# Optimization experiments

Hardware: AMD Instinct MI355X
Metric: run time of the kernel (lower is better)

The kernel has to match this reference:

```python
import jax, jax.numpy as jnp
import numpy as np

# Faithful JAX port of torchvision rotate(img, -angle, BILINEAR) applied to every
# (image, angle) pair, matching torchvision's align_corners=False grid_sample math:
# for output pixel (yo, xo), with a = radians(angle) (sign of the module's -angle
# already folded in), centered coords X = xo-(W-1)/2, Y = yo-(H-1)/2:
#   src_x = cos(a)*X - sin(a)*Y + (W-1)/2
#   src_y = sin(a)*X + cos(a)*Y + (H-1)/2
# then bilinear sample with zero padding outside the image.

def rotate_batch(image_batch, angles):
    n, c, H, W = image_batch.shape  # c == 1 (required by original output assignment)
    img = image_batch[:, 0]         # (n, H, W)
    a = jnp.deg2rad(angles)         # (k,)
    cx = (W - 1) * 0.5
    cy = (H - 1) * 0.5
    X = (jnp.arange(W, dtype=image_batch.dtype) - cx)[None, None, :]  # (1,1,W)
    Y = (jnp.arange(H, dtype=image_batch.dtype) - cy)[None, :, None]  # (1,H,1)
    ca = jnp.cos(a)[:, None, None]  # (k,1,1)
    sa = jnp.sin(a)[:, None, None]
    sx = ca * X - sa * Y + cx       # (k,H,W) source x in pixel coords
    sy = sa * X + ca * Y + cy       # (k,H,W)

    x0f = jnp.floor(sx); y0f = jnp.floor(sy)
    wx = sx - x0f; wy = sy - y0f    # bilinear fractional weights
    x0 = x0f.astype(jnp.int32); y0 = y0f.astype(jnp.int32)
    x1 = x0 + 1; y1 = y0 + 1

    def gather(yi, xi):
        # zero-padding grid_sample: out-of-bounds corners contribute 0
        valid = (yi >= 0) & (yi < H) & (xi >= 0) & (xi < W)      # (k,H,W)
        yc = jnp.clip(yi, 0, H - 1)
        xc = jnp.clip(xi, 0, W - 1)
        vals = img[:, yc, xc]                                     # (n,k,H,W)
        return jnp.where(valid[None], vals, jnp.zeros((), image_batch.dtype))

    out = (gather(y0, x0) * ((1 - wy) * (1 - wx))[None]
         + gather(y0, x1) * ((1 - wy) * wx)[None]
         + gather(y1, x0) * (wy * (1 - wx))[None]
         + gather(y1, x1) * (wy * wx)[None])
    return out  # (n, k, H, W)


def setup_inputs() -> dict:
    key = jax.random.key(0)
    k_img, k_ang = jax.random.split(key)
    image_batch = jax.random.normal(k_img, (32, 1, 512, 512), dtype=jnp.float32)
    angles = jax.random.uniform(k_ang, (8,), dtype=jnp.float32) * 360.0  # degrees
    return {"image_batch": image_batch, "angles": angles}


def reference(image_batch, angles):
    return rotate_batch(image_batch, angles)
```

## Files before the change

### kernel.cpp

```cpp
#include <hip/hip_runtime.h>
#include <math.h>
#include <stdint.h>

#define N_IMG 32
#define N_ANG 8
#define H_ 512
#define W_ 512

#define TX 64
#define TY 32
#define LP 84
#define NCHUNK 25
#define LWORDS (NCHUNK * 256)
#define OP 68

__global__ __launch_bounds__(256, 3) void rotate_tile_kernel(
    const float* __restrict__ img,
    const float* __restrict__ angles,
    float* __restrict__ out)
{
    __shared__ float tile[2 * LWORDS];

    const int bz   = blockIdx.z;
    const int k    = bz >> 1;
    const int n0   = (bz & 1) * (N_IMG / 2);
    const int tx0  = blockIdx.x * TX;
    const int ty0  = blockIdx.y * TY;
    const int tid  = threadIdx.x;
    const int wid  = tid >> 6;
    const int lane = tid & 63;

    const float rad = angles[k] * 0.017453292519943295f;
    float sa, ca;
    sincosf(rad, &sa, &ca);
    const float cx = (W_ - 1) * 0.5f;
    const float cy = (H_ - 1) * 0.5f;

    float minsx = 1e30f, maxsx = -1e30f, minsy = 1e30f, maxsy = -1e30f;
#pragma unroll
    for (int cyi = 0; cyi < 2; ++cyi) {
#pragma unroll
        for (int cxi = 0; cxi < 2; ++cxi) {
            const float xr = (float)(tx0 + cxi * (TX - 1)) - cx;
            const float yr = (float)(ty0 + cyi * (TY - 1)) - cy;
            const float sx = ca * xr - sa * yr + cx;
            const float sy = sa * xr + ca * yr + cy;
            minsx = fminf(minsx, sx); maxsx = fmaxf(maxsx, sx);
            minsy = fminf(minsy, sy); maxsy = fmaxf(maxsy, sy);
        }
    }
    const int bx0 = min(max((int)floorf(minsx) - 1, 0), W_ - 1);
    const int by0 = min(max((int)floorf(minsy) - 1, 0), H_ - 1);
    const int bx0m = (bx0 & ~3) - 4;
    const int by0m = by0 - 1;

    int goff[7];
    int nst = 0;
    for (int s = wid; s < NCHUNK; s += 4) {
        const int f   = s * 256 + lane * 4;
        const int row = f / LP;
        const int col = f - row * LP;
        const int grow = min(max(by0m + row, 0), H_ - 1);
        const int gcol = min(max(bx0m + col, 0), W_ - 4);
        goff[nst++] = grow * W_ + gcol;
    }

    const bool modeA = fabsf(ca) >= fabsf(sa);
    const int pxg = modeA ? (tid & 15) : (tid >> 4);
    const int py0 = modeA ? (tid >> 4) : (tid & 15);
    const int px  = pxg * 4;

    int   ob[2][4];
    float w00[2][4], w01[2][4], w10[2][4], w11[2][4];
#pragma unroll
    for (int p = 0; p < 2; ++p) {
        const int   yy = ty0 + py0 + p * 16;
        const float yr = (float)yy - cy;
#pragma unroll
        for (int j = 0; j < 4; ++j) {
            const int   xx = tx0 + px + j;
            const float xr = (float)xx - cx;
            const float sxs = ca * xr - sa * yr + cx;
            const float sys = sa * xr + ca * yr + cy;
            const float x0f = floorf(sxs), y0f = floorf(sys);
            const float wx = sxs - x0f, wy = sys - y0f;
            const int x0 = (int)x0f, y0 = (int)y0f;
            const bool vx0 = ((unsigned)x0       < (unsigned)W_);
            const bool vx1 = ((unsigned)(x0 + 1) < (unsigned)W_);
            const bool vy0 = ((unsigned)y0       < (unsigned)H_);
            const bool vy1 = ((unsigned)(y0 + 1) < (unsigned)H_);
            const int lx = min(max(x0 - bx0m, 0), 82);
            const int ly = min(max(y0 - by0m, 0), 74);
            ob[p][j] = ly * LP + lx;
            const float omwx = 1.0f - wx, omwy = 1.0f - wy;
            w00[p][j] = omwy * omwx * (float)(vy0 && vx0);
            w01[p][j] = omwy * wx   * (float)(vy0 && vx1);
            w10[p][j] = wy   * omwx * (float)(vy1 && vx0);
            w11[p][j] = wy   * wx   * (float)(vy1 && vx1);
        }
    }

    auto stage_img = [&](int n, int b) {
        const float* __restrict__ ib = img + (size_t)n * (H_ * W_);
        float* dst0 = &tile[b * LWORDS];
        for (int i = 0; i < nst; ++i) {
            __builtin_amdgcn_global_load_lds(
                (const __attribute__((address_space(1))) void*)(ib + goff[i]),
                (__attribute__((address_space(3))) void*)(dst0 + (wid + i * 4) * 256),
                16, 0, 0);
        }
    };

    stage_img(n0, 0);
    asm volatile("s_waitcnt vmcnt(0)" ::: "memory");
    __builtin_amdgcn_s_barrier();

    int cur = 0;
    for (int idx = 0; idx < N_IMG / 2; ++idx) {
        const int n = n0 + idx;
        const bool more = (idx + 1 < N_IMG / 2);
        if (more) {
            stage_img(n + 1, cur ^ 1);
            __builtin_amdgcn_sched_barrier(0);
        }

        const float* __restrict__ tb = &tile[cur * LWORDS];
        float* __restrict__ outn =
            out + ((size_t)(n * N_ANG + k) * H_ + ty0) * W_ + tx0;

        float v[2][4];
#pragma unroll
        for (int p = 0; p < 2; ++p) {
#pragma unroll
            for (int j = 0; j < 4; ++j) {
                const float* __restrict__ b0 = &tb[ob[p][j]];
                v[p][j] = w00[p][j] * b0[0]
                        + w01[p][j] * b0[1]
                        + w10[p][j] * b0[LP]
                        + w11[p][j] * b0[LP + 1];
            }
        }

        if (modeA) {
#pragma unroll
            for (int p = 0; p < 2; ++p) {
                float4* dst = (float4*)(outn + (py0 + p * 16) * W_ + px);
                *dst = make_float4(v[p][0], v[p][1], v[p][2], v[p][3]);
            }
        } else {
            __builtin_amdgcn_s_barrier();
            float* __restrict__ os = (float*)&tile[cur * LWORDS];
#pragma unroll
            for (int p = 0; p < 2; ++p) {
                float4* d = (float4*)(os + (py0 + p * 16) * OP + px);
                *d = make_float4(v[p][0], v[p][1], v[p][2], v[p][3]);
            }
            asm volatile("s_waitcnt lgkmcnt(0)" ::: "memory");
            __builtin_amdgcn_sched_barrier(0);
            __builtin_amdgcn_s_barrier();
            const int rx = (tid & 15) * 4;
            const int ry = tid >> 4;
#pragma unroll
            for (int p = 0; p < 2; ++p) {
                float4 t = *(float4*)(os + (ry + p * 16) * OP + rx);
                *(float4*)(outn + (ry + p * 16) * W_ + rx) = t;
            }
        }

        if (more) {
            asm volatile("s_waitcnt vmcnt(2)" ::: "memory");
            __builtin_amdgcn_s_barrier();
            cur ^= 1;
        }
    }
}

extern "C" void kernel_launch(void* const* d_in, const int* in_sizes, int n_in,
                              void* d_out, int out_size, void* d_ws, size_t ws_size,
                              hipStream_t stream) {
    const float* img    = (const float*)d_in[0];
    const float* angles = (const float*)d_in[1];
    float* out          = (float*)d_out;

    dim3 block(256, 1, 1);
    dim3 grid(W_ / TX, H_ / TY, N_ANG * 2);
    rotate_tile_kernel<<<grid, block, 0, stream>>>(img, angles, out);
}
```

Baseline: 339.3 us.

## Enlarge tiles, size LDS footprint per angle, and remap blocks across XCDs

The output tile grows from 64x32 to 64x64, and the LDS staging region is now sized from each tile's rotated bounding box instead of a fixed worst case. The double-buffered prefetch pipeline is replaced by a single buffer with a full wait per image, which frees LDS for four blocks per CU. Bilinear weights are recomputed from the fractional parts, with validity packed into bitmasks to cut register use. The grid is flattened to 1024 blocks and remapped so XCDs share angles and image halves. Output writes become nontemporal stores. The cost is that the overlap between loads and compute is lost.

```diff
diff --git a/kernel.cpp b/kernel.cpp
--- a/kernel.cpp
+++ b/kernel.cpp
@@ -8,24 +8,31 @@
 #define W_ 512
 
 #define TX 64
-#define TY 32
-#define LP 84
-#define NCHUNK 25
-#define LWORDS (NCHUNK * 256)
+#define TY 64
+#define MAXCH 37
+#define LDSW (MAXCH * 256)
 #define OP 68
 
-__global__ __launch_bounds__(256, 3) void rotate_tile_kernel(
+typedef float f32x4 __attribute__((ext_vector_type(4)));
+
+__global__ __launch_bounds__(256, 4) void rotate_tile_kernel(
     const float* __restrict__ img,
     const float* __restrict__ angles,
     float* __restrict__ out)
 {
-    __shared__ float tile[2 * LWORDS];
-
-    const int bz   = blockIdx.z;
-    const int k    = bz >> 1;
-    const int n0   = (bz & 1) * (N_IMG / 2);
-    const int tx0  = blockIdx.x * TX;
-    const int ty0  = blockIdx.y * TY;
+    __shared__ float tile[LDSW];
+
+    const int b    = blockIdx.x;
+    const int xcd  = b & 7;
+    const int slot = b >> 3;
+    const int sel  = slot & 1;
+    const int tnum = slot >> 1;
+    const int h    = xcd >> 2;
+    const int k    = (xcd & 3) + sel * 4;
+    const int n0   = h * (N_IMG / 2);
+    const int tx0  = (tnum & 7) * TX;
+    const int ty0  = (tnum >> 3) * TY;
+
     const int tid  = threadIdx.x;
     const int wid  = tid >> 6;
     const int lane = tid & 63;
@@ -51,14 +58,21 @@
     }
     const int bx0 = min(max((int)floorf(minsx) - 1, 0), W_ - 1);
     const int by0 = min(max((int)floorf(minsy) - 1, 0), H_ - 1);
-    const int bx0m = (bx0 & ~3) - 4;
-    const int by0m = by0 - 1;
-
-    int goff[7];
+    const int bx0m = (minsx < 0.0f) ? -4 : (bx0 & ~3);
+    const int by0m = (minsy < 0.0f) ? -1 : by0;
+    int cols  = (int)floorf(maxsx) + 2 - bx0m;
+    int LP    = (cols + 3) & ~3;
+    if ((LP & 7) == 0) LP += 4;
+    int rowsS = (int)floorf(maxsy) + 2 - by0m;
+    LP    = min(LP, 100);
+    rowsS = min(rowsS, 94);
+    const int nchunk = min((rowsS * LP + 255) >> 8, MAXCH);
+
+    int goff[10];
     int nst = 0;
-    for (int s = wid; s < NCHUNK; s += 4) {
-        const int f   = s * 256 + lane * 4;
-        const int row = f / LP;
+    for (int s = wid; s < nchunk; s += 4) {
+        const int f = s * 256 + lane * 4;
+        const int row = (int)((unsigned)f / (unsigned)LP);
         const int col = f - row * LP;
         const int grow = min(max(by0m + row, 0), H_ - 1);
         const int gcol = min(max(bx0m + col, 0), W_ - 4);
@@ -70,10 +84,11 @@
     const int py0 = modeA ? (tid >> 4) : (tid & 15);
     const int px  = pxg * 4;
 
-    int   ob[2][4];
-    float w00[2][4], w01[2][4], w10[2][4], w11[2][4];
-#pragma unroll
-    for (int p = 0; p < 2; ++p) {
+    int      obw[4][4];
+    float    wxv[4][4], wyv[4][4];
+    unsigned vm[2] = {0u, 0u};
+#pragma unroll
+    for (int p = 0; p < 4; ++p) {
         const int   yy = ty0 + py0 + p * 16;
         const float yr = (float)yy - cy;
 #pragma unroll
@@ -83,77 +98,88 @@
             const float sxs = ca * xr - sa * yr + cx;
             const float sys = sa * xr + ca * yr + cy;
             const float x0f = floorf(sxs), y0f = floorf(sys);
-            const float wx = sxs - x0f, wy = sys - y0f;
+            wxv[p][j] = sxs - x0f;
+            wyv[p][j] = sys - y0f;
             const int x0 = (int)x0f, y0 = (int)y0f;
-            const bool vx0 = ((unsigned)x0       < (unsigned)W_);
-            const bool vx1 = ((unsigned)(x0 + 1) < (unsigned)W_);
-            const bool vy0 = ((unsigned)y0       < (unsigned)H_);
-            const bool vy1 = ((unsigned)(y0 + 1) < (unsigned)H_);
-            const int lx = min(max(x0 - bx0m, 0), 82);
-            const int ly = min(max(y0 - by0m, 0), 74);
-            ob[p][j] = ly * LP + lx;
-            const float omwx = 1.0f - wx, omwy = 1.0f - wy;
-            w00[p][j] = omwy * omwx * (float)(vy0 && vx0);
-            w01[p][j] = omwy * wx   * (float)(vy0 && vx1);
-            w10[p][j] = wy   * omwx * (float)(vy1 && vx0);
-            w11[p][j] = wy   * wx   * (float)(vy1 && vx1);
-        }
-    }
-
-    auto stage_img = [&](int n, int b) {
+            const unsigned vx0 = ((unsigned)x0       < (unsigned)W_) ? 1u : 0u;
+            const unsigned vx1 = ((unsigned)(x0 + 1) < (unsigned)W_) ? 1u : 0u;
+            const unsigned vy0 = ((unsigned)y0       < (unsigned)H_) ? 1u : 0u;
+            const unsigned vy1 = ((unsigned)(y0 + 1) < (unsigned)H_) ? 1u : 0u;
+            const int lx = min(max(x0 - bx0m, 0), LP - 2);
+            const int ly = min(max(y0 - by0m, 0), rowsS - 2);
+            obw[p][j] = ly * LP + lx;
+            const unsigned bits = (vy0 & vx0) | ((vy0 & vx1) << 1)
+                                | ((vy1 & vx0) << 2) | ((vy1 & vx1) << 3);
+            vm[p >> 1] |= bits << ((((p & 1) << 2) + j) << 2);
+        }
+    }
+
+    for (int idx = 0; idx < N_IMG / 2; ++idx) {
+        const int n = n0 + idx;
         const float* __restrict__ ib = img + (size_t)n * (H_ * W_);
-        float* dst0 = &tile[b * LWORDS];
         for (int i = 0; i < nst; ++i) {
             __builtin_amdgcn_global_load_lds(
                 (const __attribute__((address_space(1))) void*)(ib + goff[i]),
-                (__attribute__((address_space(3))) void*)(dst0 + (wid + i * 4) * 256),
+                (__attribute__((address_space(3))) void*)(&tile[(wid + i * 4) * 256]),
                 16, 0, 0);
         }
-    };
-
-    stage_img(n0, 0);
-    asm volatile("s_waitcnt vmcnt(0)" ::: "memory");
-    __builtin_amdgcn_s_barrier();
-
-    int cur = 0;
-    for (int idx = 0; idx < N_IMG / 2; ++idx) {
-        const int n = n0 + idx;
-        const bool more = (idx + 1 < N_IMG / 2);
-        if (more) {
-            stage_img(n + 1, cur ^ 1);
-            __builtin_amdgcn_sched_barrier(0);
-        }
-
-        const float* __restrict__ tb = &tile[cur * LWORDS];
+        asm volatile("s_waitcnt vmcnt(0)" ::: "memory");
+        __builtin_amdgcn_s_barrier();
+
         float* __restrict__ outn =
             out + ((size_t)(n * N_ANG + k) * H_ + ty0) * W_ + tx0;
 
-        float v[2][4];
-#pragma unroll
-        for (int p = 0; p < 2; ++p) {
-#pragma unroll
-            for (int j = 0; j < 4; ++j) {
-                const float* __restrict__ b0 = &tb[ob[p][j]];
-                v[p][j] = w00[p][j] * b0[0]
-                        + w01[p][j] * b0[1]
-                        + w10[p][j] * b0[LP]
-                        + w11[p][j] * b0[LP + 1];
-            }
-        }
-
         if (modeA) {
 #pragma unroll
-            for (int p = 0; p < 2; ++p) {
-                float4* dst = (float4*)(outn + (py0 + p * 16) * W_ + px);
-                *dst = make_float4(v[p][0], v[p][1], v[p][2], v[p][3]);
+            for (int p = 0; p < 4; ++p) {
+                float v[4];
+#pragma unroll
+                for (int j = 0; j < 4; ++j) {
+                    const float* __restrict__ b0 = &tile[obw[p][j]];
+                    float t00 = b0[0], t01 = b0[1];
+                    float t10 = b0[LP], t11 = b0[LP + 1];
+                    const unsigned mb = vm[p >> 1] >> ((((p & 1) << 2) + j) << 2);
+                    t00 = (mb & 1u) ? t00 : 0.0f;
+                    t01 = (mb & 2u) ? t01 : 0.0f;
+                    t10 = (mb & 4u) ? t10 : 0.0f;
+                    t11 = (mb & 8u) ? t11 : 0.0f;
+                    const float wx = wxv[p][j], wy = wyv[p][j];
+                    const float omwx = 1.0f - wx, omwy = 1.0f - wy;
+                    v[j] = (omwy * omwx) * t00 + (omwy * wx) * t01
+                         + (wy * omwx) * t10 + (wy * wx) * t11;
+                }
+                f32x4 vv = { v[0], v[1], v[2], v[3] };
+                __builtin_nontemporal_store(
+                    vv, (f32x4*)(outn + (py0 + p * 16) * W_ + px));
             }
         } else {
+            float v[4][4];
+#pragma unroll
+            for (int p = 0; p < 4; ++p) {
+#pragma unroll
+                for (int j = 0; j < 4; ++j) {
+                    const float* __restrict__ b0 = &tile[obw[p][j]];
+                    float t00 = b0[0], t01 = b0[1];
+                    float t10 = b0[LP], t11 = b0[LP + 1];
+                    const unsigned mb = vm[p >> 1] >> ((((p & 1) << 2) + j) << 2);
+                    t00 = (mb & 1u) ? t00 : 0.0f;
+                    t01 = (mb & 2u) ? t01 : 0.0f;
+                    t10 = (mb & 4u) ? t10 : 0.0f;
+                    t11 = (mb & 8u) ? t11 : 0.0f;
+                    const float wx = wxv[p][j], wy = wyv[p][j];
+                    const float omwx = 1.0f - wx, omwy = 1.0f - wy;
+                    v[p][j] = (omwy * omwx) * t00 + (omwy * wx) * t01
+                            + (wy * omwx) * t10 + (wy * wx) * t11;
+                }
+            }
+            asm volatile("s_waitcnt lgkmcnt(0)" ::: "memory");
+            __builtin_amdgcn_sched_barrier(0);
             __builtin_amdgcn_s_barrier();
-            float* __restrict__ os = (float*)&tile[cur * LWORDS];
-#pragma unroll
-            for (int p = 0; p < 2; ++p) {
-                float4* d = (float4*)(os + (py0 + p * 16) * OP + px);
-                *d = make_float4(v[p][0], v[p][1], v[p][2], v[p][3]);
+            float* __restrict__ os = tile;
+#pragma unroll
+            for (int p = 0; p < 4; ++p) {
+                f32x4 vv = { v[p][0], v[p][1], v[p][2], v[p][3] };
+                *(f32x4*)(os + (py0 + p * 16) * OP + px) = vv;
             }
             asm volatile("s_waitcnt lgkmcnt(0)" ::: "memory");
             __builtin_amdgcn_sched_barrier(0);
@@ -161,17 +187,16 @@
             const int rx = (tid & 15) * 4;
             const int ry = tid >> 4;
 #pragma unroll
-            for (int p = 0; p < 2; ++p) {
-                float4 t = *(float4*)(os + (ry + p * 16) * OP + rx);
-                *(float4*)(outn + (ry + p * 16) * W_ + rx) = t;
-            }
-        }
-
-        if (more) {
-            asm volatile("s_waitcnt vmcnt(2)" ::: "memory");
-            __builtin_amdgcn_s_barrier();
-            cur ^= 1;
-        }
+            for (int p = 0; p < 4; ++p) {
+                f32x4 t = *(f32x4*)(os + (ry + p * 16) * OP + rx);
+                __builtin_nontemporal_store(
+                    t, (f32x4*)(outn + (ry + p * 16) * W_ + rx));
+            }
+        }
+
+        asm volatile("s_waitcnt lgkmcnt(0)" ::: "memory");
+        __builtin_amdgcn_sched_barrier(0);
+        __builtin_amdgcn_s_barrier();
     }
 }
 
@@ -183,6 +208,6 @@
     float* out          = (float*)d_out;
 
     dim3 block(256, 1, 1);
-    dim3 grid(W_ / TX, H_ / TY, N_ANG * 2);
+    dim3 grid(1024, 1, 1);
     rotate_tile_kernel<<<grid, block, 0, stream>>>(img, angles, out);
 }
```

Result: slower. 379.5 us (+11.9%).
